# Optimization experiments

Measured on AMD Instinct MI355X. Metric: run time of the kernel, lower is better.

The kernel has to match this reference:

```python
import jax, jax.numpy as jnp
import numpy as np

N_CH = 256          # EEG channels = graph nodes
T = 100000          # timesteps
CNN_OUT = 32
GRU_H = 64
GNN_H = 32
N_CLS = 2
THRESH = 0.7


def _conv1d(x, w, b, stride, pad):
    # x: [N, C_in, L], w: [C_out, C_in, K]
    y = jax.lax.conv_general_dilated(
        x, w, window_strides=(stride,), padding=[(pad, pad)],
        dimension_numbers=("NCH", "OIH", "NCH"))
    return y + b[None, :, None]


def _gru_last_hidden(xs, wih, whh, bih, bhh):
    # xs: [S, N, in], returns final hidden [N, H] (PyTorch GRU equations)
    H = whh.shape[1]
    h0 = jnp.zeros((xs.shape[1], H), xs.dtype)

    def step(h, x):
        gi = x @ wih.T + bih          # [N, 3H]
        gh = h @ whh.T + bhh
        i_r, i_z, i_n = jnp.split(gi, 3, axis=-1)
        h_r, h_z, h_n = jnp.split(gh, 3, axis=-1)
        r = jax.nn.sigmoid(i_r + h_r)
        z = jax.nn.sigmoid(i_z + h_z)
        n = jnp.tanh(i_n + r * h_n)
        h = (1.0 - z) * n + z * h
        return h, None

    hT, _ = jax.lax.scan(step, h0, xs)
    return hT


def _pairwise_corrcoef(x):
    x = x - x.mean(axis=1, keepdims=True)
    x = x / (x.std(axis=1, keepdims=True, ddof=1) + 1e-6)  # torch std is unbiased
    return (x @ x.T) / x.shape[1]


def _gcn(x, A_hat, w, b):
    # PyG GCNConv: A_hat @ (x @ W^T) + b  (sym-normalized adj w/ self-loops)
    return A_hat @ (x @ w.T) + b


def setup_inputs() -> dict:
    key = jax.random.key(0)
    ks = jax.random.split(key, 24)
    r = lambda i, shape, s: (jax.random.normal(ks[i], shape, jnp.float32) * s)
    d = {
        "data": r(0, (N_CH, T), 1.0),
        "conv1_w": r(1, (8, 1, 11), 0.3), "conv1_b": r(2, (8,), 0.1),
        "conv2_w": r(3, (16, 8, 7), 0.1), "conv2_b": r(4, (16,), 0.1),
        "conv3_w": r(5, (CNN_OUT, 16, 5), 0.1), "conv3_b": r(6, (CNN_OUT,), 0.1),
        "gru_wih_f": r(7, (3 * GRU_H, CNN_OUT), 0.1), "gru_whh_f": r(8, (3 * GRU_H, GRU_H), 0.1),
        "gru_bih_f": r(9, (3 * GRU_H,), 0.05), "gru_bhh_f": r(10, (3 * GRU_H,), 0.05),
        "gru_wih_b": r(11, (3 * GRU_H, CNN_OUT), 0.1), "gru_whh_b": r(12, (3 * GRU_H, GRU_H), 0.1),
        "gru_bih_b": r(13, (3 * GRU_H,), 0.05), "gru_bhh_b": r(14, (3 * GRU_H,), 0.05),
        "gcn1_w": r(15, (GNN_H, 2 * GRU_H), 0.1), "gcn1_b": r(16, (GNN_H,), 0.05),
        "gcn2_w": r(17, (GNN_H, GNN_H), 0.15), "gcn2_b": r(18, (GNN_H,), 0.05),
        "cls_w": r(19, (N_CLS, GNN_H), 0.15), "cls_b": r(20, (N_CLS,), 0.05),
    }
    return d


def reference(data, conv1_w, conv1_b, conv2_w, conv2_b, conv3_w, conv3_b,
              gru_wih_f, gru_whh_f, gru_bih_f, gru_bhh_f,
              gru_wih_b, gru_whh_b, gru_bih_b, gru_bhh_b,
              gcn1_w, gcn1_b, gcn2_w, gcn2_b, cls_w, cls_b):
    x = data[:, None, :]                                 # [N, 1, T]
    x = jax.nn.relu(_conv1d(x, conv1_w, conv1_b, 5, 5))  # [N, 8, 20000]
    x = jax.nn.relu(_conv1d(x, conv2_w, conv2_b, 5, 3))  # [N, 16, 4000]
    x = jax.nn.relu(_conv1d(x, conv3_w, conv3_b, 5, 2))  # [N, 32, 800]
    xs = jnp.transpose(x, (2, 0, 1))                     # [S=800, N, 32]

    h_f = _gru_last_hidden(xs, gru_wih_f, gru_whh_f, gru_bih_f, gru_bhh_f)
    h_b = _gru_last_hidden(xs[::-1], gru_wih_b, gru_whh_b, gru_bih_b, gru_bhh_b)
    # torch h_n.permute(1,0,2).reshape(N,-1) -> concat [fwd, bwd]
    h_n = jnp.concatenate([h_f, h_b], axis=-1)           # [N, 128]

    corr = _pairwise_corrcoef(h_n)                       # [N, N]
    # dense adjacency = thresholded |corr|; diagonal is ~1 so self-loops present
    # (matches PyG add_remaining_self_loops: already there). Always nonempty.
    A = (jnp.abs(corr) > THRESH).astype(h_n.dtype)
    deg = A.sum(axis=1)
    dinv = jax.lax.rsqrt(jnp.maximum(deg, 1e-12))
    A_hat = A * dinv[:, None] * dinv[None, :]            # D^-1/2 A D^-1/2

    h = jax.nn.relu(_gcn(h_n, A_hat, gcn1_w, gcn1_b))
    h = jax.nn.relu(_gcn(h, A_hat, gcn2_w, gcn2_b))
    graph_emb = h.mean(axis=0, keepdims=True)            # [1, GNN_H]
    return graph_emb @ cls_w.T + cls_b                   # [1, N_CLS]
```

## Files before the change

kernel.cpp:

```cpp
#include <hip/hip_runtime.h>
#include <math.h>

#define N_CH 256
#define T_IN 100000
#define L1O 20000
#define L2O 4000
#define L3O 800
#define C1 8
#define C2 16
#define C3 32

#define TILE3 25
#define NY2   125
#define NY1   627
#define ND    3141

#define KEEP1(x) asm volatile("" : "+v"(x))

__device__ __forceinline__ float sigm(float x) {
    x = fminf(fmaxf(x, -30.0f), 30.0f);
    return 1.0f / (1.0f + __expf(-x));
}
__device__ __forceinline__ float tanhfast(float x) {
    x = fminf(fmaxf(x, -15.0f), 15.0f);
    float e = __expf(-2.0f * x);
    return (1.0f - e) / (1.0f + e);
}
__device__ __forceinline__ float dot4(float4 a, float4 b) {
    return a.x * b.x + a.y * b.y + a.z * b.z + a.w * b.w;
}
__device__ __forceinline__ float bcast(float v, int lane) {
    return __int_as_float(__builtin_amdgcn_readlane(__float_as_int(v), lane));
}

__global__ __launch_bounds__(256) void k_conv(
    const float* __restrict__ data,
    const float* __restrict__ w1, const float* __restrict__ b1,
    const float* __restrict__ w2, const float* __restrict__ b2,
    const float* __restrict__ w3, const float* __restrict__ b3,
    float* __restrict__ x3)
{
    __shared__ __align__(16) float sd[ND];
    __shared__ __align__(16) float sy1[NY1][C1];
    __shared__ __align__(16) float sy2[NY2][C2];
    __shared__ __align__(16) float sw1[C1 * 11];
    __shared__ float sb1[C1];
    __shared__ __align__(16) float sw2[C2 * C1 * 7];
    __shared__ float sb2[C2];
    __shared__ __align__(16) float sw3[C3 * C2 * 5];
    __shared__ float sb3[C3];

    const int tid = threadIdx.x;
    const int tb  = blockIdx.x;
    const int ch  = blockIdx.y;
    const int t0    = tb * TILE3;
    const int dbase = 3125 * tb - 70;
    const int ubase = 625 * tb - 13;
    const int sbase = 125 * tb - 2;

    for (int e = tid; e < C1 * 11;    e += 256) sw1[e] = w1[e];
    for (int e = tid; e < C1;         e += 256) sb1[e] = b1[e];
    for (int e = tid; e < C2 * C1 * 7; e += 256) sw2[e] = w2[e];
    for (int e = tid; e < C2;         e += 256) sb2[e] = b2[e];
    for (int e = tid; e < C3 * C2 * 5; e += 256) sw3[e] = w3[e];
    for (int e = tid; e < C3;         e += 256) sb3[e] = b3[e];

    const float* dch = data + (size_t)ch * T_IN;
    for (int e = tid; e < ND; e += 256) {
        int g = dbase + e;
        sd[e] = (g >= 0 && g < T_IN) ? dch[g] : 0.0f;
    }
    __syncthreads();

    {
        const int c = tid & 7;
        float wr[11];
        #pragma unroll
        for (int k = 0; k < 11; ++k) wr[k] = sw1[c * 11 + k];
        const float bb = sb1[c];
        for (int u = tid >> 3; u < NY1; u += 32) {
            int ug = ubase + u;
            float acc = bb;
            #pragma unroll
            for (int k = 0; k < 11; ++k) acc += wr[k] * sd[5 * u + k];
            sy1[u][c] = (ug >= 0 && ug < L1O) ? fmaxf(acc, 0.0f) : 0.0f;
        }
    }
    __syncthreads();

    {
        const int c = tid & 15;
        float wr[56];
        #pragma unroll
        for (int q = 0; q < 14; ++q)
            ((float4*)wr)[q] = ((const float4*)(sw2 + c * 56))[q];
        const float bb = sb2[c];
        for (int s = tid >> 4; s < NY2; s += 16) {
            int sg = sbase + s;
            float acc = bb;
            #pragma unroll
            for (int k = 0; k < 7; ++k) {
                const float4* y4 = (const float4*)&sy1[5 * s + k][0];
                float4 ya = y4[0], yb = y4[1];
                acc += wr[0*7+k]*ya.x + wr[1*7+k]*ya.y + wr[2*7+k]*ya.z + wr[3*7+k]*ya.w
                     + wr[4*7+k]*yb.x + wr[5*7+k]*yb.y + wr[6*7+k]*yb.z + wr[7*7+k]*yb.w;
            }
            sy2[s][c] = (sg >= 0 && sg < L2O) ? fmaxf(acc, 0.0f) : 0.0f;
        }
    }
    __syncthreads();

    {
        const int o = tid & 31;
        float wr[80];
        #pragma unroll
        for (int q = 0; q < 20; ++q)
            ((float4*)wr)[q] = ((const float4*)(sw3 + o * 80))[q];
        const float bb = sb3[o];
        for (int tl = tid >> 5; tl < TILE3; tl += 8) {
            float acc = bb;
            #pragma unroll
            for (int k = 0; k < 5; ++k) {
                const float4* y4 = (const float4*)&sy2[5 * tl + k][0];
                float4 za = y4[0], zb = y4[1], zc = y4[2], zd = y4[3];
                acc += wr[0*5+k]*za.x  + wr[1*5+k]*za.y  + wr[2*5+k]*za.z  + wr[3*5+k]*za.w
                     + wr[4*5+k]*zb.x  + wr[5*5+k]*zb.y  + wr[6*5+k]*zb.z  + wr[7*5+k]*zb.w
                     + wr[8*5+k]*zc.x  + wr[9*5+k]*zc.y  + wr[10*5+k]*zc.z + wr[11*5+k]*zc.w
                     + wr[12*5+k]*zd.x + wr[13*5+k]*zd.y + wr[14*5+k]*zd.z + wr[15*5+k]*zd.w;
            }
            x3[((size_t)ch * L3O + (t0 + tl)) * C3 + o] = fmaxf(acc, 0.0f);
        }
    }
}

__global__ __launch_bounds__(192, 1) void k_gru4(
    const float* __restrict__ x3,
    const float* __restrict__ wih_f, const float* __restrict__ bih_f,
    const float* __restrict__ whh_f, const float* __restrict__ bhh_f,
    const float* __restrict__ wih_b, const float* __restrict__ bih_b,
    const float* __restrict__ whh_b, const float* __restrict__ bhh_b,
    float* __restrict__ hN)
{
    const int tid  = threadIdx.x;
    const int lane = tid & 63;
    const int g    = tid >> 6;
    const int ch = blockIdx.x, dir = blockIdx.y;
    const float* wih = dir ? wih_b : wih_f;
    const float* whh = dir ? whh_b : whh_f;
    const float* bih = dir ? bih_b : bih_f;
    const float* bhh = dir ? bhh_b : bhh_f;
    const int row = g * 64 + lane;

    __shared__ float sdot[2][4][64];

    float w[64];
    {
        const float4* w4 = (const float4*)(whh + row * 64);
        #pragma unroll
        for (int q = 0; q < 16; ++q) {
            float4 v = w4[q];
            w[4*q] = v.x; w[4*q+1] = v.y; w[4*q+2] = v.z; w[4*q+3] = v.w;
        }
    }
    float wi[32];
    {
        const float4* w4 = (const float4*)(wih + row * 32);
        #pragma unroll
        for (int q = 0; q < 8; ++q) {
            float4 v = w4[q];
            wi[4*q] = v.x; wi[4*q+1] = v.y; wi[4*q+2] = v.z; wi[4*q+3] = v.w;
        }
    }
    #pragma unroll
    for (int j = 0; j < 64; ++j) KEEP1(w[j]);
    #pragma unroll
    for (int j = 0; j < 32; ++j) KEEP1(wi[j]);

    const float bi = bih[row];
    const float bh = bhh[row];

    const float* xp = x3 + (size_t)ch * L3O * 32 + (lane & 31);
    const int xstride = dir ? -32 : 32;
    if (dir) xp += (size_t)(L3O - 1) * 32;

    float x0 = xp[0]; xp += xstride;
    float x1 = xp[0]; xp += xstride;
    float x2 = xp[0]; xp += xstride;

    float h = 0.0f;

    for (int s = 0; s < L3O; ++s) {
        float xnext = 0.0f;
        if (s + 3 < L3O) xnext = xp[0];
        xp += xstride;

        float a0 = bi, a0b = 0.0f;
        #pragma unroll
        for (int k = 0; k < 32; k += 2) {
            a0  = fmaf(wi[k],     bcast(x0, k),     a0);
            a0b = fmaf(wi[k + 1], bcast(x0, k + 1), a0b);
        }
        float a1 = bh, a1b = 0.0f, a1c = 0.0f, a1d = 0.0f;
        #pragma unroll
        for (int j = 0; j < 64; j += 4) {
            a1  = fmaf(w[j],     bcast(h, j),     a1);
            a1b = fmaf(w[j + 1], bcast(h, j + 1), a1b);
            a1c = fmaf(w[j + 2], bcast(h, j + 2), a1c);
            a1d = fmaf(w[j + 3], bcast(h, j + 3), a1d);
        }
        float ai = a0 + a0b;
        float ah = (a1 + a1b) + (a1c + a1d);

        const int p = s & 1;
        if (g < 2) {
            sdot[p][g][lane] = ai + ah;
        } else {
            sdot[p][2][lane] = ah;
            sdot[p][3][lane] = ai;
        }
        __syncthreads();

        float sr  = sdot[p][0][lane];
        float sz  = sdot[p][1][lane];
        float shn = sdot[p][2][lane];
        float sin_= sdot[p][3][lane];
        float r = sigm(sr);
        float z = sigm(sz);
        float n = tanhfast(sin_ + r * shn);
        h = (1.0f - z) * n + z * h;

        x0 = x1; x1 = x2; x2 = xnext;
    }
    if (g == 0) hN[ch * 128 + dir * 64 + lane] = h;
}

__global__ __launch_bounds__(128) void k_norm(
    const float* __restrict__ hN, const float* __restrict__ gcn1_w,
    float* __restrict__ Xn, float* __restrict__ XnT, float* __restrict__ hw1)
{
    const int i = blockIdx.x, tid = threadIdx.x;
    __shared__ float red[128];
    __shared__ float row[128];
    float v = hN[i * 128 + tid];
    row[tid] = v;
    red[tid] = v;
    __syncthreads();
    for (int s = 64; s > 0; s >>= 1) { if (tid < s) red[tid] += red[tid + s]; __syncthreads(); }
    float mean = red[0] / 128.0f;
    __syncthreads();
    float d = v - mean;
    red[tid] = d * d;
    __syncthreads();
    for (int s = 64; s > 0; s >>= 1) { if (tid < s) red[tid] += red[tid + s]; __syncthreads(); }
    float sd = sqrtf(red[0] / 127.0f);
    float xn = d / (sd + 1e-6f);
    Xn[i * 128 + tid] = xn;
    XnT[tid * 256 + i] = xn;
    if (tid < 32) {
        float acc = 0.f;
        for (int k = 0; k < 128; ++k) acc += row[k] * gcn1_w[tid * 128 + k];
        hw1[i * 32 + tid] = acc;
    }
}

__global__ __launch_bounds__(256) void k_corr(
    const float* __restrict__ Xn, const float* __restrict__ XnT,
    float* __restrict__ A, float* __restrict__ deg)
{
    const int i = blockIdx.x, tid = threadIdx.x;
    __shared__ float xi[128];
    __shared__ float red[256];
    if (tid < 128) xi[tid] = Xn[i * 128 + tid];
    __syncthreads();
    float c = 0.f;
    for (int k = 0; k < 128; ++k) c += xi[k] * XnT[k * 256 + tid];
    c *= (1.0f / 128.0f);
    float a = (fabsf(c) > 0.7f) ? 1.0f : 0.0f;
    A[i * 256 + tid] = a;
    red[tid] = a;
    __syncthreads();
    for (int s = 128; s > 0; s >>= 1) { if (tid < s) red[tid] += red[tid + s]; __syncthreads(); }
    if (tid == 0) deg[i] = red[0];
}

__global__ __launch_bounds__(256) void k_gcn(
    const float* __restrict__ A, const float* __restrict__ deg,
    const float* __restrict__ hw, const float* __restrict__ bias,
    const float* __restrict__ wNext,
    float* __restrict__ hOut, float* __restrict__ hwNext)
{
    const int i = blockIdx.x, tid = threadIdx.x;
    const int f = tid & 31, grp = tid >> 5;
    __shared__ float aj[256];
    __shared__ float red[8][32];
    __shared__ float hrow[32];
    float dj = rsqrtf(fmaxf(deg[tid], 1e-12f));
    aj[tid] = A[i * 256 + tid] * dj;
    __syncthreads();
    float p = 0.f;
    for (int j = grp * 32; j < grp * 32 + 32; ++j) p += aj[j] * hw[j * 32 + f];
    red[grp][f] = p;
    __syncthreads();
    if (grp == 0) {
        float s = 0.f;
        #pragma unroll
        for (int g = 0; g < 8; ++g) s += red[g][f];
        float di = rsqrtf(fmaxf(deg[i], 1e-12f));
        float o = fmaxf(bias[f] + di * s, 0.0f);
        hOut[i * 32 + f] = o;
        hrow[f] = o;
    }
    __syncthreads();
    if (wNext != nullptr && grp == 0) {
        float acc = 0.f;
        #pragma unroll
        for (int k = 0; k < 32; ++k) acc += hrow[k] * wNext[f * 32 + k];
        hwNext[i * 32 + f] = acc;
    }
}

__global__ __launch_bounds__(64) void k_head(
    const float* __restrict__ h2, const float* __restrict__ cls_w,
    const float* __restrict__ cls_b, float* __restrict__ out)
{
    const int tid = threadIdx.x;
    __shared__ float mean[32];
    if (tid < 32) {
        float s = 0.f;
        for (int i = 0; i < 256; ++i) s += h2[i * 32 + tid];
        mean[tid] = s * (1.0f / 256.0f);
    }
    __syncthreads();
    if (tid < 2) {
        float s = cls_b[tid];
        #pragma unroll
        for (int fe = 0; fe < 32; ++fe) s += mean[fe] * cls_w[tid * 32 + fe];
        out[tid] = s;
    }
}

extern "C" void kernel_launch(void* const* d_in, const int* in_sizes, int n_in,
                              void* d_out, int out_size, void* d_ws, size_t ws_size,
                              hipStream_t stream) {
    const float* data    = (const float*)d_in[0];
    const float* conv1_w = (const float*)d_in[1];
    const float* conv1_b = (const float*)d_in[2];
    const float* conv2_w = (const float*)d_in[3];
    const float* conv2_b = (const float*)d_in[4];
    const float* conv3_w = (const float*)d_in[5];
    const float* conv3_b = (const float*)d_in[6];
    const float* wih_f   = (const float*)d_in[7];
    const float* whh_f   = (const float*)d_in[8];
    const float* bih_f   = (const float*)d_in[9];
    const float* bhh_f   = (const float*)d_in[10];
    const float* wih_b   = (const float*)d_in[11];
    const float* whh_b   = (const float*)d_in[12];
    const float* bih_b   = (const float*)d_in[13];
    const float* bhh_b   = (const float*)d_in[14];
    const float* gcn1_w  = (const float*)d_in[15];
    const float* gcn1_b  = (const float*)d_in[16];
    const float* gcn2_w  = (const float*)d_in[17];
    const float* gcn2_b  = (const float*)d_in[18];
    const float* cls_w   = (const float*)d_in[19];
    const float* cls_b   = (const float*)d_in[20];

    float* ws  = (float*)d_ws;
    float* x3  = ws;
    float* hN  = x3 + 6553600;
    float* Xn  = hN + 32768;
    float* XnT = Xn + 32768;
    float* A   = XnT + 32768;
    float* deg = A + 65536;
    float* hw1 = deg + 256;
    float* h1  = hw1 + 8192;
    float* hw2 = h1 + 8192;
    float* h2  = hw2 + 8192;

    k_conv<<<dim3(32, 256), 256, 0, stream>>>(data, conv1_w, conv1_b, conv2_w, conv2_b,
                                              conv3_w, conv3_b, x3);
    k_gru4<<<dim3(256, 2), 192, 0, stream>>>(x3, wih_f, bih_f, whh_f, bhh_f,
                                             wih_b, bih_b, whh_b, bhh_b, hN);
    k_norm<<<256, 128, 0, stream>>>(hN, gcn1_w, Xn, XnT, hw1);
    k_corr<<<256, 256, 0, stream>>>(Xn, XnT, A, deg);
    k_gcn<<<256, 256, 0, stream>>>(A, deg, hw1, gcn1_b, gcn2_w, h1, hw2);
    k_gcn<<<256, 256, 0, stream>>>(A, deg, hw2, gcn2_b, nullptr, h2, nullptr);
    k_head<<<1, 64, 0, stream>>>(h2, cls_w, cls_b, (float*)d_out);
}
```

Measured before the change: 1.195 ms.

## Split GRU recurrence over K across four waves and rework conv stages

The GRU kernel now uses four wavefronts that each own a 16-wide slice of the hidden-state reduction for all three gates, so each lane does 48 FMAs per step instead of 96. Partial sums are reduced through shared memory once per step, which shortens the serial chain per timestep at the cost of extra LDS traffic. The conv kernel no longer stages weights in shared memory; weights are read directly as uniform global loads. Each thread now computes all output channels for one position, reusing input values held in registers.

```diff
diff --git a/kernel.cpp b/kernel.cpp
--- a/kernel.cpp
+++ b/kernel.cpp
@@ -15,8 +15,6 @@
 #define NY1   627
 #define ND    3141
 
-#define KEEP1(x) asm volatile("" : "+v"(x))
-
 __device__ __forceinline__ float sigm(float x) {
     x = fminf(fmaxf(x, -30.0f), 30.0f);
     return 1.0f / (1.0f + __expf(-x));
@@ -26,11 +24,11 @@
     float e = __expf(-2.0f * x);
     return (1.0f - e) / (1.0f + e);
 }
-__device__ __forceinline__ float dot4(float4 a, float4 b) {
-    return a.x * b.x + a.y * b.y + a.z * b.z + a.w * b.w;
-}
 __device__ __forceinline__ float bcast(float v, int lane) {
     return __int_as_float(__builtin_amdgcn_readlane(__float_as_int(v), lane));
+}
+__device__ __forceinline__ float f4e(const float4& v, int e) {
+    return ((const float*)&v)[e];
 }
 
 __global__ __launch_bounds__(256) void k_conv(
@@ -43,12 +41,6 @@
     __shared__ __align__(16) float sd[ND];
     __shared__ __align__(16) float sy1[NY1][C1];
     __shared__ __align__(16) float sy2[NY2][C2];
-    __shared__ __align__(16) float sw1[C1 * 11];
-    __shared__ float sb1[C1];
-    __shared__ __align__(16) float sw2[C2 * C1 * 7];
-    __shared__ float sb2[C2];
-    __shared__ __align__(16) float sw3[C3 * C2 * 5];
-    __shared__ float sb3[C3];
 
     const int tid = threadIdx.x;
     const int tb  = blockIdx.x;
@@ -58,13 +50,6 @@
     const int ubase = 625 * tb - 13;
     const int sbase = 125 * tb - 2;
 
-    for (int e = tid; e < C1 * 11;    e += 256) sw1[e] = w1[e];
-    for (int e = tid; e < C1;         e += 256) sb1[e] = b1[e];
-    for (int e = tid; e < C2 * C1 * 7; e += 256) sw2[e] = w2[e];
-    for (int e = tid; e < C2;         e += 256) sb2[e] = b2[e];
-    for (int e = tid; e < C3 * C2 * 5; e += 256) sw3[e] = w3[e];
-    for (int e = tid; e < C3;         e += 256) sb3[e] = b3[e];
-
     const float* dch = data + (size_t)ch * T_IN;
     for (int e = tid; e < ND; e += 256) {
         int g = dbase + e;
@@ -72,68 +57,103 @@
     }
     __syncthreads();
 
+    for (int u = tid; u < NY1; u += 256) {
+        int ug = ubase + u;
+        bool ok = (ug >= 0 && ug < L1O);
+        float t[11];
+        #pragma unroll
+        for (int k = 0; k < 11; ++k) t[k] = sd[5 * u + k];
+        float acc[8];
+        #pragma unroll
+        for (int c = 0; c < 8; ++c) acc[c] = b1[c];
+        #pragma unroll
+        for (int k = 0; k < 11; ++k) {
+            float tv = t[k];
+            #pragma unroll
+            for (int c = 0; c < 8; ++c) acc[c] = fmaf(w1[c * 11 + k], tv, acc[c]);
+        }
+        float4 o0, o1;
+        o0.x = ok ? fmaxf(acc[0], 0.f) : 0.f;  o0.y = ok ? fmaxf(acc[1], 0.f) : 0.f;
+        o0.z = ok ? fmaxf(acc[2], 0.f) : 0.f;  o0.w = ok ? fmaxf(acc[3], 0.f) : 0.f;
+        o1.x = ok ? fmaxf(acc[4], 0.f) : 0.f;  o1.y = ok ? fmaxf(acc[5], 0.f) : 0.f;
+        o1.z = ok ? fmaxf(acc[6], 0.f) : 0.f;  o1.w = ok ? fmaxf(acc[7], 0.f) : 0.f;
+        ((float4*)&sy1[u][0])[0] = o0;
+        ((float4*)&sy1[u][0])[1] = o1;
+    }
+    __syncthreads();
+
     {
-        const int c = tid & 7;
-        float wr[11];
-        #pragma unroll
-        for (int k = 0; k < 11; ++k) wr[k] = sw1[c * 11 + k];
-        const float bb = sb1[c];
-        for (int u = tid >> 3; u < NY1; u += 32) {
-            int ug = ubase + u;
-            float acc = bb;
-            #pragma unroll
-            for (int k = 0; k < 11; ++k) acc += wr[k] * sd[5 * u + k];
-            sy1[u][c] = (ug >= 0 && ug < L1O) ? fmaxf(acc, 0.0f) : 0.0f;
+        const int s    = tid & 127;
+        const int half = tid >> 7;
+        if (s < NY2) {
+            int sg = sbase + s;
+            bool ok = (sg >= 0 && sg < L2O);
+            float tp[56];
+            #pragma unroll
+            for (int k = 0; k < 7; ++k) {
+                float4 a = ((const float4*)&sy1[5 * s + k][0])[0];
+                float4 b = ((const float4*)&sy1[5 * s + k][0])[1];
+                tp[k * 8 + 0] = a.x; tp[k * 8 + 1] = a.y; tp[k * 8 + 2] = a.z; tp[k * 8 + 3] = a.w;
+                tp[k * 8 + 4] = b.x; tp[k * 8 + 5] = b.y; tp[k * 8 + 6] = b.z; tp[k * 8 + 7] = b.w;
+            }
+            const int c0 = half * 8;
+            float acc[8];
+            #pragma unroll
+            for (int cc = 0; cc < 8; ++cc) acc[cc] = b2[c0 + cc];
+            #pragma unroll
+            for (int cc = 0; cc < 8; ++cc) {
+                const float* wp = w2 + (c0 + cc) * 56;
+                float a = acc[cc];
+                #pragma unroll
+                for (int ci = 0; ci < 8; ++ci)
+                    #pragma unroll
+                    for (int k = 0; k < 7; ++k)
+                        a = fmaf(wp[ci * 7 + k], tp[k * 8 + ci], a);
+                acc[cc] = a;
+            }
+            float4 o0, o1;
+            o0.x = ok ? fmaxf(acc[0], 0.f) : 0.f;  o0.y = ok ? fmaxf(acc[1], 0.f) : 0.f;
+            o0.z = ok ? fmaxf(acc[2], 0.f) : 0.f;  o0.w = ok ? fmaxf(acc[3], 0.f) : 0.f;
+            o1.x = ok ? fmaxf(acc[4], 0.f) : 0.f;  o1.y = ok ? fmaxf(acc[5], 0.f) : 0.f;
+            o1.z = ok ? fmaxf(acc[6], 0.f) : 0.f;  o1.w = ok ? fmaxf(acc[7], 0.f) : 0.f;
+            ((float4*)&sy2[s][c0])[0] = o0;
+            ((float4*)&sy2[s][c0])[1] = o1;
         }
     }
     __syncthreads();
 
     {
-        const int c = tid & 15;
-        float wr[56];
-        #pragma unroll
-        for (int q = 0; q < 14; ++q)
-            ((float4*)wr)[q] = ((const float4*)(sw2 + c * 56))[q];
-        const float bb = sb2[c];
-        for (int s = tid >> 4; s < NY2; s += 16) {
-            int sg = sbase + s;
-            float acc = bb;
-            #pragma unroll
-            for (int k = 0; k < 7; ++k) {
-                const float4* y4 = (const float4*)&sy1[5 * s + k][0];
-                float4 ya = y4[0], yb = y4[1];
-                acc += wr[0*7+k]*ya.x + wr[1*7+k]*ya.y + wr[2*7+k]*ya.z + wr[3*7+k]*ya.w
-                     + wr[4*7+k]*yb.x + wr[5*7+k]*yb.y + wr[6*7+k]*yb.z + wr[7*7+k]*yb.w;
-            }
-            sy2[s][c] = (sg >= 0 && sg < L2O) ? fmaxf(acc, 0.0f) : 0.0f;
+        const int s    = tid & 127;
+        const int half = tid >> 7;
+        if (s < TILE3) {
+            float tp[80];
+            #pragma unroll
+            for (int k = 0; k < 5; ++k) {
+                #pragma unroll
+                for (int q = 0; q < 4; ++q) {
+                    float4 a = ((const float4*)&sy2[5 * s + k][0])[q];
+                    tp[k * 16 + q * 4 + 0] = a.x; tp[k * 16 + q * 4 + 1] = a.y;
+                    tp[k * 16 + q * 4 + 2] = a.z; tp[k * 16 + q * 4 + 3] = a.w;
+                }
+            }
+            const int o0 = half * 16;
+            float* xo = x3 + ((size_t)ch * L3O + (t0 + s)) * C3 + o0;
+            #pragma unroll
+            for (int oo = 0; oo < 16; ++oo) {
+                const float* wp = w3 + (o0 + oo) * 80;
+                float a = b3[o0 + oo];
+                #pragma unroll
+                for (int ci = 0; ci < 16; ++ci)
+                    #pragma unroll
+                    for (int k = 0; k < 5; ++k)
+                        a = fmaf(wp[ci * 5 + k], tp[k * 16 + ci], a);
+                xo[oo] = fmaxf(a, 0.f);
+            }
         }
     }
-    __syncthreads();
-
-    {
-        const int o = tid & 31;
-        float wr[80];
-        #pragma unroll
-        for (int q = 0; q < 20; ++q)
-            ((float4*)wr)[q] = ((const float4*)(sw3 + o * 80))[q];
-        const float bb = sb3[o];
-        for (int tl = tid >> 5; tl < TILE3; tl += 8) {
-            float acc = bb;
-            #pragma unroll
-            for (int k = 0; k < 5; ++k) {
-                const float4* y4 = (const float4*)&sy2[5 * tl + k][0];
-                float4 za = y4[0], zb = y4[1], zc = y4[2], zd = y4[3];
-                acc += wr[0*5+k]*za.x  + wr[1*5+k]*za.y  + wr[2*5+k]*za.z  + wr[3*5+k]*za.w
-                     + wr[4*5+k]*zb.x  + wr[5*5+k]*zb.y  + wr[6*5+k]*zb.z  + wr[7*5+k]*zb.w
-                     + wr[8*5+k]*zc.x  + wr[9*5+k]*zc.y  + wr[10*5+k]*zc.z + wr[11*5+k]*zc.w
-                     + wr[12*5+k]*zd.x + wr[13*5+k]*zd.y + wr[14*5+k]*zd.z + wr[15*5+k]*zd.w;
-            }
-            x3[((size_t)ch * L3O + (t0 + tl)) * C3 + o] = fmaxf(acc, 0.0f);
-        }
-    }
-}
-
-__global__ __launch_bounds__(192, 1) void k_gru4(
+}
+
+__global__ __launch_bounds__(256) void k_gru5(
     const float* __restrict__ x3,
     const float* __restrict__ wih_f, const float* __restrict__ bih_f,
     const float* __restrict__ whh_f, const float* __restrict__ bhh_f,
@@ -141,97 +161,95 @@
     const float* __restrict__ whh_b, const float* __restrict__ bhh_b,
     float* __restrict__ hN)
 {
-    const int tid  = threadIdx.x;
-    const int lane = tid & 63;
-    const int g    = tid >> 6;
+    const int tid = threadIdx.x;
+    const int l   = tid & 63;
+    const int w   = tid >> 6;
     const int ch = blockIdx.x, dir = blockIdx.y;
     const float* wih = dir ? wih_b : wih_f;
     const float* whh = dir ? whh_b : whh_f;
     const float* bih = dir ? bih_b : bih_f;
     const float* bhh = dir ? bhh_b : bhh_f;
-    const int row = g * 64 + lane;
-
-    __shared__ float sdot[2][4][64];
-
-    float w[64];
-    {
-        const float4* w4 = (const float4*)(whh + row * 64);
-        #pragma unroll
-        for (int q = 0; q < 16; ++q) {
-            float4 v = w4[q];
-            w[4*q] = v.x; w[4*q+1] = v.y; w[4*q+2] = v.z; w[4*q+3] = v.w;
-        }
-    }
-    float wi[32];
-    {
-        const float4* w4 = (const float4*)(wih + row * 32);
-        #pragma unroll
-        for (int q = 0; q < 8; ++q) {
-            float4 v = w4[q];
-            wi[4*q] = v.x; wi[4*q+1] = v.y; wi[4*q+2] = v.z; wi[4*q+3] = v.w;
-        }
-    }
+
+    __shared__ float sdot[2][4][4][64];
+
+    float4 whq[12];
     #pragma unroll
-    for (int j = 0; j < 64; ++j) KEEP1(w[j]);
+    for (int g = 0; g < 3; ++g)
+        #pragma unroll
+        for (int q = 0; q < 4; ++q)
+            whq[g * 4 + q] = *(const float4*)&whh[(g * 64 + l) * 64 + w * 16 + q * 4];
+    float4 wiq[6];
     #pragma unroll
-    for (int j = 0; j < 32; ++j) KEEP1(wi[j]);
-
-    const float bi = bih[row];
-    const float bh = bhh[row];
-
-    const float* xp = x3 + (size_t)ch * L3O * 32 + (lane & 31);
+    for (int g = 0; g < 3; ++g)
+        #pragma unroll
+        for (int q = 0; q < 2; ++q)
+            wiq[g * 2 + q] = *(const float4*)&wih[(g * 64 + l) * 32 + w * 8 + q * 4];
+
+    const float br   = bih[l] + bhh[l];
+    const float bz   = bih[64 + l] + bhh[64 + l];
+    const float bin_ = bih[128 + l];
+    const float bhn  = bhh[128 + l];
+
+    const float* xp = x3 + (size_t)ch * L3O * 32 + (l & 31);
     const int xstride = dir ? -32 : 32;
     if (dir) xp += (size_t)(L3O - 1) * 32;
-
     float x0 = xp[0]; xp += xstride;
     float x1 = xp[0]; xp += xstride;
     float x2 = xp[0]; xp += xstride;
 
     float h = 0.0f;
+    const int kb = w * 16;
+    const int xb = w * 8;
 
     for (int s = 0; s < L3O; ++s) {
-        float xnext = 0.0f;
-        if (s + 3 < L3O) xnext = xp[0];
+        float xn_ = 0.0f;
+        if (s + 3 < L3O) xn_ = xp[0];
         xp += xstride;
 
-        float a0 = bi, a0b = 0.0f;
-        #pragma unroll
-        for (int k = 0; k < 32; k += 2) {
-            a0  = fmaf(wi[k],     bcast(x0, k),     a0);
-            a0b = fmaf(wi[k + 1], bcast(x0, k + 1), a0b);
+        float pr = 0.f, pz = 0.f, pn = 0.f;
+        #pragma unroll
+        for (int q = 0; q < 4; ++q)
+            #pragma unroll
+            for (int e = 0; e < 4; ++e) {
+                float hb = bcast(h, kb + q * 4 + e);
+                pr = fmaf(f4e(whq[q],     e), hb, pr);
+                pz = fmaf(f4e(whq[4 + q], e), hb, pz);
+                pn = fmaf(f4e(whq[8 + q], e), hb, pn);
+            }
+        float ir = 0.f, iz = 0.f, in_ = 0.f;
+        #pragma unroll
+        for (int q = 0; q < 2; ++q)
+            #pragma unroll
+            for (int e = 0; e < 4; ++e) {
+                float xv = bcast(x0, xb + q * 4 + e);
+                ir  = fmaf(f4e(wiq[q],     e), xv, ir);
+                iz  = fmaf(f4e(wiq[2 + q], e), xv, iz);
+                in_ = fmaf(f4e(wiq[4 + q], e), xv, in_);
+            }
+
+        const int p = s & 1;
+        sdot[p][w][0][l] = pr + ir;
+        sdot[p][w][1][l] = pz + iz;
+        sdot[p][w][2][l] = pn;
+        sdot[p][w][3][l] = in_;
+        __syncthreads();
+
+        float sr = br, sz_ = bz, snh = bhn, sni = bin_;
+        #pragma unroll
+        for (int ww = 0; ww < 4; ++ww) {
+            sr  += sdot[p][ww][0][l];
+            sz_ += sdot[p][ww][1][l];
+            snh += sdot[p][ww][2][l];
+            sni += sdot[p][ww][3][l];
         }
-        float a1 = bh, a1b = 0.0f, a1c = 0.0f, a1d = 0.0f;
-        #pragma unroll
-        for (int j = 0; j < 64; j += 4) {
-            a1  = fmaf(w[j],     bcast(h, j),     a1);
-            a1b = fmaf(w[j + 1], bcast(h, j + 1), a1b);
-            a1c = fmaf(w[j + 2], bcast(h, j + 2), a1c);
-            a1d = fmaf(w[j + 3], bcast(h, j + 3), a1d);
-        }
-        float ai = a0 + a0b;
-        float ah = (a1 + a1b) + (a1c + a1d);
-
-        const int p = s & 1;
-        if (g < 2) {
-            sdot[p][g][lane] = ai + ah;
-        } else {
-            sdot[p][2][lane] = ah;
-            sdot[p][3][lane] = ai;
-        }
-        __syncthreads();
-
-        float sr  = sdot[p][0][lane];
-        float sz  = sdot[p][1][lane];
-        float shn = sdot[p][2][lane];
-        float sin_= sdot[p][3][lane];
         float r = sigm(sr);
-        float z = sigm(sz);
-        float n = tanhfast(sin_ + r * shn);
+        float z = sigm(sz_);
+        float n = tanhfast(sni + r * snh);
         h = (1.0f - z) * n + z * h;
 
-        x0 = x1; x1 = x2; x2 = xnext;
-    }
-    if (g == 0) hN[ch * 128 + dir * 64 + lane] = h;
+        x0 = x1; x1 = x2; x2 = xn_;
+    }
+    if (w == 0) hN[ch * 128 + dir * 64 + l] = h;
 }
 
 __global__ __launch_bounds__(128) void k_norm(
@@ -378,7 +396,7 @@
 
     k_conv<<<dim3(32, 256), 256, 0, stream>>>(data, conv1_w, conv1_b, conv2_w, conv2_b,
                                               conv3_w, conv3_b, x3);
-    k_gru4<<<dim3(256, 2), 192, 0, stream>>>(x3, wih_f, bih_f, whh_f, bhh_f,
+    k_gru5<<<dim3(256, 2), 256, 0, stream>>>(x3, wih_f, bih_f, whh_f, bhh_f,
                                              wih_b, bih_b, whh_b, bhh_b, hN);
     k_norm<<<256, 128, 0, stream>>>(hN, gcn1_w, Xn, XnT, hw1);
     k_corr<<<256, 256, 0, stream>>>(Xn, XnT, A, deg);
```

After: 1.093 ms. -8.5%, faster.
